# Optimization experiments

Measured on AMD Instinct MI355X. Metric: run time of the kernel, lower is better.

## Reference

```python
import jax, jax.numpy as jnp
import numpy as np
from jax import lax

INPUT_DIM = 16
H1 = 5
H2 = 50
NUM_CLASSES = 20
B = 4096
T = 512


def _lstm(x, w_ih, w_hh, b_ih, b_hh, hidden):
    # x: [B, T, D]; PyTorch LSTM gate order i, f, g, o; returns all hidden states [B, T, H]
    xg = jnp.einsum('btd,gd->btg', x, w_ih) + (b_ih + b_hh)  # [B, T, 4H]
    xg_t = jnp.swapaxes(xg, 0, 1)  # [T, B, 4H]
    h0 = jnp.zeros((x.shape[0], hidden), x.dtype)
    c0 = jnp.zeros((x.shape[0], hidden), x.dtype)

    def step(carry, xt):
        h, c = carry
        g = xt + h @ w_hh.T  # [B, 4H]
        i, f, gg, o = jnp.split(g, 4, axis=-1)
        i = jax.nn.sigmoid(i)
        f = jax.nn.sigmoid(f)
        gg = jnp.tanh(gg)
        o = jax.nn.sigmoid(o)
        c = f * c + i * gg
        h = o * jnp.tanh(c)
        return (h, c), h

    _, hs = lax.scan(step, (h0, c0), xg_t)
    return jnp.swapaxes(hs, 0, 1)  # [B, T, H]


def setup_inputs() -> dict:
    key = jax.random.key(0)
    ks = jax.random.split(key, 12)
    s1 = 1.0 / np.sqrt(H1)
    s2 = 1.0 / np.sqrt(H2)
    u = lambda k, shape, s: jax.random.uniform(k, shape, jnp.float32, -s, s)
    return {
        'x': jax.random.normal(ks[0], (B, T, INPUT_DIM), jnp.float32),
        'w_ih1': u(ks[1], (4 * H1, INPUT_DIM), s1),
        'w_hh1': u(ks[2], (4 * H1, H1), s1),
        'b_ih1': u(ks[3], (4 * H1,), s1),
        'b_hh1': u(ks[4], (4 * H1,), s1),
        'w_ih2': u(ks[5], (4 * H2, H1), s2),
        'w_hh2': u(ks[6], (4 * H2, H2), s2),
        'b_ih2': u(ks[7], (4 * H2,), s2),
        'b_hh2': u(ks[8], (4 * H2,), s2),
        'fc_w': u(ks[9], (NUM_CLASSES, H2), s2),
        'fc_b': u(ks[10], (NUM_CLASSES,), s2),
    }


def reference(x, w_ih1, w_hh1, b_ih1, b_hh1, w_ih2, w_hh2, b_ih2, b_hh2, fc_w, fc_b):
    h1 = _lstm(x, w_ih1, w_hh1, b_ih1, b_hh1, H1)   # [B, T, 5]
    h2 = _lstm(h1, w_ih2, w_hh2, b_ih2, b_hh2, H2)  # [B, T, 50]
    feat = h2[:, -1, :]  # last timestep; dropout is identity in eval mode
    out = feat @ fc_w.T + fc_b  # [B, num_classes]
    return (out, feat)
```

## Files before the change

### kernel.cpp

```cpp
#include <hip/hip_runtime.h>
#include <stdint.h>

#define B_TOTAL 4096
#define T_STEPS 512
#define IN_DIM 16
#define H1 5
#define H2 50
#define NCLS 20

typedef __attribute__((ext_vector_type(8))) short bf16x8;
typedef __attribute__((ext_vector_type(4))) float f32x4;

#define LOG2E 1.44269504f
__device__ inline float sigm(float x){
  float e = __builtin_amdgcn_exp2f(-LOG2E * x);
  return __builtin_amdgcn_rcpf(1.0f + e);
}
__device__ inline float tanh_(float x){
  float e = __builtin_amdgcn_exp2f((2.0f*LOG2E) * x);
  float r = __builtin_amdgcn_rcpf(1.0f + e);
  return fmaf(-2.0f, r, 1.0f);
}
__device__ inline unsigned pack_top(float a, float b){
  return __builtin_amdgcn_perm(__float_as_uint(a), __float_as_uint(b), 0x07060302u);
}
__device__ inline void cvt_store(unsigned short* dh, unsigned short* dl, float4 v){
  uint2 H, L;
  H.x = pack_top(v.y, v.x);
  H.y = pack_top(v.w, v.z);
  float r0 = v.x - __uint_as_float(__float_as_uint(v.x) & 0xFFFF0000u);
  float r1 = v.y - __uint_as_float(__float_as_uint(v.y) & 0xFFFF0000u);
  float r2 = v.z - __uint_as_float(__float_as_uint(v.z) & 0xFFFF0000u);
  float r3 = v.w - __uint_as_float(__float_as_uint(v.w) & 0xFFFF0000u);
  L.x = pack_top(r1, r0);
  L.y = pack_top(r3, r2);
  *(uint2*)dh = H; *(uint2*)dl = L;
}
__device__ inline void split1(float h, unsigned short& hi, unsigned short& lo){
  unsigned u = __float_as_uint(h);
  hi = (unsigned short)(u >> 16);
  float r = h - __uint_as_float(u & 0xFFFF0000u);
  lo = (unsigned short)(__float_as_uint(r) >> 16);
}
__device__ inline void wsplit(float w, short& hi, short& lo){
  unsigned u = __float_as_uint(w);
  hi = (short)(u >> 16);
  float r = w - __uint_as_float(u & 0xFFFF0000u);
  lo = (short)(__float_as_uint(r) >> 16);
}

#define LDS_FENCE() __asm__ volatile("s_waitcnt lgkmcnt(0)" ::: "memory")
#define BARRIER()   __asm__ volatile("s_barrier" ::: "memory")

__global__ __launch_bounds__(320, 1) void lstm_fused_kernel(
    const float* __restrict__ x,
    const float* __restrict__ w_ih1, const float* __restrict__ w_hh1,
    const float* __restrict__ b_ih1, const float* __restrict__ b_hh1,
    const float* __restrict__ w_ih2, const float* __restrict__ w_hh2,
    const float* __restrict__ b_ih2, const float* __restrict__ b_hh2,
    const float* __restrict__ fc_w, const float* __restrict__ fc_b,
    float* __restrict__ out)
{
  const int tid  = threadIdx.x;
  const int lane = tid & 63;
  const int wave = tid >> 6;
  const int l15  = lane & 15;
  const int quad = lane >> 4;
  const int b0   = blockIdx.x * 16;

  __shared__ __align__(16) unsigned short a2h[2][16*72], a2l[2][16*72];
  __shared__ __align__(16) unsigned short xrh[8][16*24], xrl[8][16*24];
  __shared__ __align__(16) unsigned short a1h[16*24], a1l[16*24];
  __shared__ float h2f[16*52];

  bf16x8 Bh[4][2], Bl[4][2];
  float bias[4];
  float cst[4] = {0.f,0.f,0.f,0.f};
  const int cg = wave*16 + l15;

  if (wave < 4){
    bool valid = cg < H2;
#pragma unroll
    for (int tt=0; tt<4; ++tt){
      int grow = tt*H2 + cg;
#pragma unroll
      for (int kt=0; kt<2; ++kt){
#pragma unroll
        for (int j=0;j<8;j++){
          int kk = kt*32 + quad*8 + j;
          float w = 0.f;
          if (valid){
            if (kk < H2)         w = w_hh2[grow*H2 + kk];
            else if (kk < H2+H1) w = w_ih2[grow*H1 + (kk-H2)];
          }
          short hi, lo; wsplit(w, hi, lo);
          Bh[tt][kt][j] = hi; Bl[tt][kt][j] = lo;
        }
      }
      bias[tt] = valid ? (b_ih2[grow] + b_hh2[grow]) : 0.f;
    }
  } else {
    bool valid = l15 < H1;
#pragma unroll
    for (int tt=0; tt<4; ++tt){
      int grow = tt*H1 + l15;
#pragma unroll
      for (int j=0;j<8;j++){
        int kk = quad*8 + j;
        float w = 0.f;
        if (valid){
          if (kk < IN_DIM)         w = w_ih1[grow*IN_DIM + kk];
          else if (kk < IN_DIM+H1) w = w_hh1[grow*H1 + (kk-IN_DIM)];
        }
        short hi, lo; wsplit(w, hi, lo);
        Bh[tt][0][j] = hi; Bl[tt][0][j] = lo;
        Bh[tt][1][j] = 0;  Bl[tt][1][j] = 0;
      }
      bias[tt] = valid ? (b_ih1[grow] + b_hh1[grow]) : 0.f;
    }
  }

  { unsigned short* p = &a2h[0][0]; for (int i=tid;i<2*16*72;i+=320) p[i]=0; }
  { unsigned short* p = &a2l[0][0]; for (int i=tid;i<2*16*72;i+=320) p[i]=0; }
  { unsigned short* p = &a1h[0];    for (int i=tid;i<16*24;i+=320)   p[i]=0; }
  { unsigned short* p = &a1l[0];    for (int i=tid;i<16*24;i+=320)   p[i]=0; }

  const int xb = lane >> 2;
  const int xd = (lane & 3) * 4;
  if (wave == 4){
#pragma unroll
    for (int s=0;s<8;s++){
      float4 v = *(const float4*)&x[((size_t)(b0+xb)*T_STEPS + s)*IN_DIM + xd];
      cvt_store(&xrh[s][xb*24+xd], &xrl[s][xb*24+xd], v);
    }
  }
  __syncthreads();

  float4 pf0, pf1, pf2, pf3;
  bool pend = false;

  for (int t=-1; t<T_STEPS; ++t){
    const int rd = t & 1;
    const int wr = rd ^ 1;

    if (wave == 4){
      const int s = t + 1;
      if (s < T_STEPS){
        if ((s & 3) == 0 && s+4 < T_STEPS){
          const float* xp = &x[((size_t)(b0+xb)*T_STEPS + (s+4))*IN_DIM + xd];
          pf0 = *(const float4*)(xp + 0*IN_DIM);
          pf1 = *(const float4*)(xp + 1*IN_DIM);
          pf2 = *(const float4*)(xp + 2*IN_DIM);
          pf3 = *(const float4*)(xp + 3*IN_DIM);
          pend = true;
        }
        const int slot = s & 7;
        bf16x8 ah, al;
        if (quad < 2){
          ah = *(const bf16x8*)&xrh[slot][l15*24 + quad*8];
          al = *(const bf16x8*)&xrl[slot][l15*24 + quad*8];
        } else {
          ah = *(const bf16x8*)&a1h[l15*24 + (quad-2)*8];
          al = *(const bf16x8*)&a1l[l15*24 + (quad-2)*8];
        }
        f32x4 acc[4];
#pragma unroll
        for (int tt=0; tt<4; ++tt){
          f32x4 cA = {bias[tt],bias[tt],bias[tt],bias[tt]};
          cA = __builtin_amdgcn_mfma_f32_16x16x32_bf16(ah, Bh[tt][0], cA, 0,0,0);
          f32x4 cB = {0.f,0.f,0.f,0.f};
          cB = __builtin_amdgcn_mfma_f32_16x16x32_bf16(al, Bh[tt][0], cB, 0,0,0);
          cB = __builtin_amdgcn_mfma_f32_16x16x32_bf16(ah, Bl[tt][0], cB, 0,0,0);
          acc[tt] = cA + cB;
        }
#pragma unroll
        for (int r=0;r<4;r++){
          float gi = sigm(acc[0][r]);
          float gf = sigm(acc[1][r]);
          float gg = tanh_(acc[2][r]);
          float go = sigm(acc[3][r]);
          cst[r] = gf*cst[r] + gi*gg;
          float h = go * tanh_(cst[r]);
          if (l15 < H1){
            unsigned short hh, hl; split1(h, hh, hl);
            int row = quad*4 + r;
            a1h[row*24 + l15] = hh;
            a1l[row*24 + l15] = hl;
            a2h[wr][row*72 + H2 + l15] = hh;
            a2l[wr][row*72 + H2 + l15] = hl;
          }
        }
        if ((s & 3) == 2 && pend){
          cvt_store(&xrh[(s+2)&7][xb*24+xd], &xrl[(s+2)&7][xb*24+xd], pf0);
          cvt_store(&xrh[(s+3)&7][xb*24+xd], &xrl[(s+3)&7][xb*24+xd], pf1);
          cvt_store(&xrh[(s+4)&7][xb*24+xd], &xrl[(s+4)&7][xb*24+xd], pf2);
          cvt_store(&xrh[(s+5)&7][xb*24+xd], &xrl[(s+5)&7][xb*24+xd], pf3);
          pend = false;
        }
      }
    } else if (t >= 0){
      const int rb = l15*72;
      bf16x8 ah0 = *(const bf16x8*)&a2h[rd][rb +      quad*8];
      bf16x8 al0 = *(const bf16x8*)&a2l[rd][rb +      quad*8];
      bf16x8 ah1 = *(const bf16x8*)&a2h[rd][rb + 32 + quad*8];
      bf16x8 al1 = *(const bf16x8*)&a2l[rd][rb + 32 + quad*8];

      f32x4 acc[4];
#pragma unroll
      for (int tt=0; tt<4; ++tt){
        f32x4 c0 = {bias[tt],bias[tt],bias[tt],bias[tt]};
        c0 = __builtin_amdgcn_mfma_f32_16x16x32_bf16(ah0, Bh[tt][0], c0, 0,0,0);
        c0 = __builtin_amdgcn_mfma_f32_16x16x32_bf16(al0, Bh[tt][0], c0, 0,0,0);
        f32x4 c1 = {0.f,0.f,0.f,0.f};
        c1 = __builtin_amdgcn_mfma_f32_16x16x32_bf16(ah0, Bl[tt][0], c1, 0,0,0);
        c1 = __builtin_amdgcn_mfma_f32_16x16x32_bf16(ah1, Bh[tt][1], c1, 0,0,0);
        f32x4 c2 = {0.f,0.f,0.f,0.f};
        c2 = __builtin_amdgcn_mfma_f32_16x16x32_bf16(al1, Bh[tt][1], c2, 0,0,0);
        c2 = __builtin_amdgcn_mfma_f32_16x16x32_bf16(ah1, Bl[tt][1], c2, 0,0,0);
        acc[tt] = (c0 + c1) + c2;
      }
      const bool act = cg < H2;
#pragma unroll
      for (int r=0;r<4;r++){
        float gi = sigm(acc[0][r]);
        float gf = sigm(acc[1][r]);
        float gg = tanh_(acc[2][r]);
        float go = sigm(acc[3][r]);
        cst[r] = gf*cst[r] + gi*gg;
        float h = go * tanh_(cst[r]);
        if (act){
          unsigned short hh, hl; split1(h, hh, hl);
          int row = quad*4 + r;
          a2h[wr][row*72 + cg] = hh;
          a2l[wr][row*72 + cg] = hl;
          if (t == T_STEPS-1){
            out[(size_t)B_TOTAL*NCLS + (size_t)(b0+row)*H2 + cg] = h;
            h2f[row*52 + cg] = h;
          }
        }
      }
    }

    LDS_FENCE();
    BARRIER();
  }

  __syncthreads();
  {
    int b = tid / 20, o = tid % 20;
    float s = fc_b[o];
#pragma unroll 10
    for (int k=0;k<H2;k++) s += fc_w[o*H2+k] * h2f[b*52+k];
    out[(size_t)(b0+b)*NCLS + o] = s;
  }
}

extern "C" void kernel_launch(void* const* d_in, const int* in_sizes, int n_in,
                              void* d_out, int out_size, void* d_ws, size_t ws_size,
                              hipStream_t stream) {
  const float* x     = (const float*)d_in[0];
  const float* w_ih1 = (const float*)d_in[1];
  const float* w_hh1 = (const float*)d_in[2];
  const float* b_ih1 = (const float*)d_in[3];
  const float* b_hh1 = (const float*)d_in[4];
  const float* w_ih2 = (const float*)d_in[5];
  const float* w_hh2 = (const float*)d_in[6];
  const float* b_ih2 = (const float*)d_in[7];
  const float* b_hh2 = (const float*)d_in[8];
  const float* fc_w  = (const float*)d_in[9];
  const float* fc_b  = (const float*)d_in[10];
  float* out = (float*)d_out;

  lstm_fused_kernel<<<dim3(B_TOTAL/16), dim3(320), 0, stream>>>(
      x, w_ih1, w_hh1, b_ih1, b_hh1, w_ih2, w_hh2, b_ih2, b_hh2, fc_w, fc_b, out);
}
```

Baseline: 723.0 us.

## Replace per-step block barriers with LDS tag-based point-to-point wave synchronization

Drops the per-timestep s_waitcnt plus s_barrier and uses per-wave read/write tags in LDS. Each wave publishes progress with a release store and spins on the minimum of the other waves' tags. Waves can now run their MFMA and activation work before waiting, and only wait for readers before overwriting the double buffer. This is meant to take barrier overhead and lockstep stalls off the serial recurrence. It also regroups the MFMA accumulators into two chains instead of three. The cost is spin-polling on LDS atomics and a correctness risk from relaxed loads with no acquire fence.

Measured after the change: 746.2 us. +3.2%, slower.

```diff
diff --git a/kernel.cpp b/kernel.cpp
--- a/kernel.cpp
+++ b/kernel.cpp
@@ -49,8 +49,24 @@
   lo = (short)(__float_as_uint(r) >> 16);
 }
 
-#define LDS_FENCE() __asm__ volatile("s_waitcnt lgkmcnt(0)" ::: "memory")
-#define BARRIER()   __asm__ volatile("s_barrier" ::: "memory")
+__device__ inline void wait_ge(unsigned* tags, unsigned tgt){
+  for(;;){
+    unsigned m0 = __hip_atomic_load(&tags[0], __ATOMIC_RELAXED, __HIP_MEMORY_SCOPE_WORKGROUP);
+    unsigned m1 = __hip_atomic_load(&tags[1], __ATOMIC_RELAXED, __HIP_MEMORY_SCOPE_WORKGROUP);
+    unsigned m2 = __hip_atomic_load(&tags[2], __ATOMIC_RELAXED, __HIP_MEMORY_SCOPE_WORKGROUP);
+    unsigned m3 = __hip_atomic_load(&tags[3], __ATOMIC_RELAXED, __HIP_MEMORY_SCOPE_WORKGROUP);
+    unsigned m4 = __hip_atomic_load(&tags[4], __ATOMIC_RELAXED, __HIP_MEMORY_SCOPE_WORKGROUP);
+    unsigned a = m0 < m1 ? m0 : m1;
+    unsigned b = m2 < m3 ? m2 : m3;
+    unsigned c = a < b ? a : b;
+    unsigned mn = c < m4 ? c : m4;
+    if (mn >= tgt) return;
+  }
+}
+__device__ inline void tag_pub(unsigned* p, unsigned v, int lane){
+  if (lane == 0)
+    __hip_atomic_store(p, v, __ATOMIC_RELEASE, __HIP_MEMORY_SCOPE_WORKGROUP);
+}
 
 __global__ __launch_bounds__(320, 1) void lstm_fused_kernel(
     const float* __restrict__ x,
@@ -72,6 +88,7 @@
   __shared__ __align__(16) unsigned short xrh[8][16*24], xrl[8][16*24];
   __shared__ __align__(16) unsigned short a1h[16*24], a1l[16*24];
   __shared__ float h2f[16*52];
+  __shared__ unsigned wtag[8], rtag[8];
 
   bf16x8 Bh[4][2], Bl[4][2];
   float bias[4];
@@ -124,6 +141,7 @@
   { unsigned short* p = &a2l[0][0]; for (int i=tid;i<2*16*72;i+=320) p[i]=0; }
   { unsigned short* p = &a1h[0];    for (int i=tid;i<16*24;i+=320)   p[i]=0; }
   { unsigned short* p = &a1l[0];    for (int i=tid;i<16*24;i+=320)   p[i]=0; }
+  if (tid < 8){ wtag[tid] = 0; rtag[tid] = 0; }
 
   const int xb = lane >> 2;
   const int xd = (lane & 3) * 4;
@@ -136,16 +154,15 @@
   }
   __syncthreads();
 
-  float4 pf0, pf1, pf2, pf3;
+  float4 pf0 = make_float4(0,0,0,0), pf1 = pf0, pf2 = pf0, pf3 = pf0;
   bool pend = false;
 
-  for (int t=-1; t<T_STEPS; ++t){
-    const int rd = t & 1;
-    const int wr = rd ^ 1;
-
-    if (wave == 4){
-      const int s = t + 1;
-      if (s < T_STEPS){
+  if (wave == 4){
+    for (int u=0; u<=T_STEPS; ++u){
+      const int wr = u & 1;
+      tag_pub(&rtag[4], (unsigned)(u+1), lane);
+      if (u < T_STEPS){
+        const int s = u;
         if ((s & 3) == 0 && s+4 < T_STEPS){
           const float* xp = &x[((size_t)(b0+xb)*T_STEPS + (s+4))*IN_DIM + xd];
           pf0 = *(const float4*)(xp + 0*IN_DIM);
@@ -173,6 +190,7 @@
           cB = __builtin_amdgcn_mfma_f32_16x16x32_bf16(ah, Bl[tt][0], cB, 0,0,0);
           acc[tt] = cA + cB;
         }
+        float hs[4];
 #pragma unroll
         for (int r=0;r<4;r++){
           float gi = sigm(acc[0][r]);
@@ -180,9 +198,13 @@
           float gg = tanh_(acc[2][r]);
           float go = sigm(acc[3][r]);
           cst[r] = gf*cst[r] + gi*gg;
-          float h = go * tanh_(cst[r]);
+          hs[r] = go * tanh_(cst[r]);
+        }
+        wait_ge(rtag, (unsigned)u);
+#pragma unroll
+        for (int r=0;r<4;r++){
           if (l15 < H1){
-            unsigned short hh, hl; split1(h, hh, hl);
+            unsigned short hh, hl; split1(hs[r], hh, hl);
             int row = quad*4 + r;
             a1h[row*24 + l15] = hh;
             a1l[row*24 + l15] = hl;
@@ -198,51 +220,64 @@
           pend = false;
         }
       }
-    } else if (t >= 0){
-      const int rb = l15*72;
-      bf16x8 ah0 = *(const bf16x8*)&a2h[rd][rb +      quad*8];
-      bf16x8 al0 = *(const bf16x8*)&a2l[rd][rb +      quad*8];
-      bf16x8 ah1 = *(const bf16x8*)&a2h[rd][rb + 32 + quad*8];
-      bf16x8 al1 = *(const bf16x8*)&a2l[rd][rb + 32 + quad*8];
-
-      f32x4 acc[4];
-#pragma unroll
-      for (int tt=0; tt<4; ++tt){
-        f32x4 c0 = {bias[tt],bias[tt],bias[tt],bias[tt]};
-        c0 = __builtin_amdgcn_mfma_f32_16x16x32_bf16(ah0, Bh[tt][0], c0, 0,0,0);
-        c0 = __builtin_amdgcn_mfma_f32_16x16x32_bf16(al0, Bh[tt][0], c0, 0,0,0);
-        f32x4 c1 = {0.f,0.f,0.f,0.f};
-        c1 = __builtin_amdgcn_mfma_f32_16x16x32_bf16(ah0, Bl[tt][0], c1, 0,0,0);
-        c1 = __builtin_amdgcn_mfma_f32_16x16x32_bf16(ah1, Bh[tt][1], c1, 0,0,0);
-        f32x4 c2 = {0.f,0.f,0.f,0.f};
-        c2 = __builtin_amdgcn_mfma_f32_16x16x32_bf16(al1, Bh[tt][1], c2, 0,0,0);
-        c2 = __builtin_amdgcn_mfma_f32_16x16x32_bf16(ah1, Bl[tt][1], c2, 0,0,0);
-        acc[tt] = (c0 + c1) + c2;
+      tag_pub(&wtag[4], (unsigned)(u+1), lane);
+    }
+  } else {
+    const bool act = cg < H2;
+    const int rb = l15*72;
+    for (int u=0; u<=T_STEPS; ++u){
+      const int rd = (u+1) & 1, wr = u & 1;
+      if (u >= 1){
+        const int t = u - 1;
+        wait_ge(wtag, (unsigned)u);
+        bf16x8 ah0 = *(const bf16x8*)&a2h[rd][rb +      quad*8];
+        bf16x8 al0 = *(const bf16x8*)&a2l[rd][rb +      quad*8];
+        bf16x8 ah1 = *(const bf16x8*)&a2h[rd][rb + 32 + quad*8];
+        bf16x8 al1 = *(const bf16x8*)&a2l[rd][rb + 32 + quad*8];
+        tag_pub(&rtag[wave], (unsigned)(u+1), lane);
+
+        f32x4 acc[4];
+#pragma unroll
+        for (int tt=0; tt<4; ++tt){
+          f32x4 c0 = {bias[tt],bias[tt],bias[tt],bias[tt]};
+          c0 = __builtin_amdgcn_mfma_f32_16x16x32_bf16(ah0, Bh[tt][0], c0, 0,0,0);
+          c0 = __builtin_amdgcn_mfma_f32_16x16x32_bf16(al0, Bh[tt][0], c0, 0,0,0);
+          c0 = __builtin_amdgcn_mfma_f32_16x16x32_bf16(ah0, Bl[tt][0], c0, 0,0,0);
+          f32x4 c1 = {0.f,0.f,0.f,0.f};
+          c1 = __builtin_amdgcn_mfma_f32_16x16x32_bf16(ah1, Bh[tt][1], c1, 0,0,0);
+          c1 = __builtin_amdgcn_mfma_f32_16x16x32_bf16(al1, Bh[tt][1], c1, 0,0,0);
+          c1 = __builtin_amdgcn_mfma_f32_16x16x32_bf16(ah1, Bl[tt][1], c1, 0,0,0);
+          acc[tt] = c0 + c1;
+        }
+        float hs[4];
+#pragma unroll
+        for (int r=0;r<4;r++){
+          float gi = sigm(acc[0][r]);
+          float gf = sigm(acc[1][r]);
+          float gg = tanh_(acc[2][r]);
+          float go = sigm(acc[3][r]);
+          cst[r] = gf*cst[r] + gi*gg;
+          hs[r] = go * tanh_(cst[r]);
+        }
+        wait_ge(rtag, (unsigned)u);
+#pragma unroll
+        for (int r=0;r<4;r++){
+          if (act){
+            unsigned short hh, hl; split1(hs[r], hh, hl);
+            int row = quad*4 + r;
+            a2h[wr][row*72 + cg] = hh;
+            a2l[wr][row*72 + cg] = hl;
+            if (t == T_STEPS-1){
+              out[(size_t)B_TOTAL*NCLS + (size_t)(b0+row)*H2 + cg] = hs[r];
+              h2f[row*52 + cg] = hs[r];
+            }
+          }
+        }
+      } else {
+        tag_pub(&rtag[wave], 1u, lane);
       }
-      const bool act = cg < H2;
-#pragma unroll
-      for (int r=0;r<4;r++){
-        float gi = sigm(acc[0][r]);
-        float gf = sigm(acc[1][r]);
-        float gg = tanh_(acc[2][r]);
-        float go = sigm(acc[3][r]);
-        cst[r] = gf*cst[r] + gi*gg;
-        float h = go * tanh_(cst[r]);
-        if (act){
-          unsigned short hh, hl; split1(h, hh, hl);
-          int row = quad*4 + r;
-          a2h[wr][row*72 + cg] = hh;
-          a2l[wr][row*72 + cg] = hl;
-          if (t == T_STEPS-1){
-            out[(size_t)B_TOTAL*NCLS + (size_t)(b0+row)*H2 + cg] = h;
-            h2f[row*52 + cg] = h;
-          }
-        }
-      }
-    }
-
-    LDS_FENCE();
-    BARRIER();
+      tag_pub(&wtag[wave], (unsigned)(u+1), lane);
+    }
   }
 
   __syncthreads();
```
